# Kernel tuning notes

Measured on AMD Instinct MI355X. Metric: run time of the kernel, lower is better.

Reference implementation:

```python
import jax, jax.numpy as jnp
import numpy as np

N = 512      # nodes
E = 16384    # edges (avg degree 32)
D = 128      # indim
OUT = 128    # outdim


def setup_inputs() -> dict:
    key = jax.random.key(0)
    k1, k2, k3 = jax.random.split(key, 3)
    X = jax.random.normal(k1, (N, N, D), dtype=jnp.float32)
    edge_index = jax.random.randint(k2, (2, E), 0, N, dtype=jnp.int64)
    W = jax.random.normal(k3, (3 * D, OUT), dtype=jnp.float32) * (1.0 / np.sqrt(3 * D))
    b = jnp.zeros((OUT,), dtype=jnp.float32)
    return {"X": X, "edge_index": edge_index, "W": W, "b": b}


def reference(X, edge_index, W, b):
    # X: [N, N, D] tuple features X[i, j] for (subgraph root i, node j)
    # edge_index: [2, E] directed edges (src -> dst), aggr = 'sum'
    n = X.shape[0]
    src, dst = edge_index[0], edge_index[1]
    # Dense binary adjacency (sum aggregation counts multi-edges, matching
    # scatter-add over the edge list). A[k, j] = #edges k -> j.
    A = jnp.zeros((n, n), dtype=X.dtype).at[src, dst].add(jnp.ones((src.shape[0],), X.dtype))
    # OpMessagePassingOnSubg2D: within subgraph i, aggregate over neighbors of j
    # X1[i, j] = sum_{k in N(j)} X[i, k]
    X1 = jnp.einsum('kj,ikd->ijd', A, X)
    # OpMessagePassingCrossSubg2D: across subgraphs, aggregate over neighbors of i
    # X2[i, j] = sum_{k in N(i)} X[k, j]
    X2 = jnp.einsum('ki,kjd->ijd', A, X)
    # catvalue([X1, X2]) -> [X, X1, X2], then pointwise MLP (single Linear)
    H = jnp.concatenate([X, X1, X2], axis=-1)  # [N, N, 3D]
    return H @ W + b  # [N, N, OUT]
```

## Files before the change

kernel.cpp:

```cpp
#include <hip/hip_runtime.h>
#include <hip/hip_bf16.h>
#include <stdint.h>

#define NN 512
#define DD 128
#define EE 16384

typedef short bf16x8 __attribute__((ext_vector_type(8)));
typedef short bf16x4 __attribute__((ext_vector_type(4)));
typedef float f32x4  __attribute__((ext_vector_type(4)));
typedef unsigned int u32;

__device__ __forceinline__ short f2bf(float f) {
    union { __hip_bfloat16 h; short s; } u;
    u.h = __float2bfloat16(f);
    return u.s;
}
__device__ __forceinline__ u32 pk2(float a, float b) {
    return (u32)(unsigned short)f2bf(a) | ((u32)(unsigned short)f2bf(b) << 16);
}

typedef __attribute__((address_space(3))) unsigned int lds_u32;
typedef __attribute__((address_space(1))) const unsigned int glb_u32;
__device__ __forceinline__ void gll16(void* l, const void* g) {
    __builtin_amdgcn_global_load_lds((glb_u32*)g, (lds_u32*)l, 16, 0, 0);
}


__global__ void k_zero(float* __restrict__ At) {
    At[blockIdx.x * 256 + threadIdx.x] = 0.0f;
}

__global__ void k_edges(const int* __restrict__ ei, float* __restrict__ At) {
    __shared__ int flag;
    if (threadIdx.x == 0) flag = 0;
    __syncthreads();
    int any = 0;
    for (int i = threadIdx.x; i < EE; i += blockDim.x) any |= ei[2 * i + 1];
    if (any) atomicOr(&flag, 1);
    __syncthreads();
    const bool is32 = (flag != 0);
    for (int e = threadIdx.x; e < EE; e += blockDim.x) {
        int src, dst;
        if (is32) { src = ei[e];     dst = ei[EE + e]; }
        else      { src = ei[2 * e]; dst = ei[2 * (EE + e)]; }
        atomicAdd(&At[dst * NN + src], 1.0f);
    }
}

__global__ void k_wt2(const float* __restrict__ W, short* __restrict__ Wt2) {
    int t = blockIdx.x * 256 + threadIdx.x;
    int kk = t >> 7, n = t & 127;
    int s = kk >> 7, d = kk & 127;
    Wt2[s * 16384 + n * 128 + d] = f2bf(W[t]);
}

__global__ void k_pack_at(const float* __restrict__ At, short* __restrict__ Atp) {
    int t = blockIdx.x * 256 + threadIdx.x;
    int T = t >> 6, l = t & 63;
    int row = (T >> 4) * 16 + (l & 15);
    int col = (T & 15) * 32 + (l >> 4) * 8;
    const float* s = &At[row * 512 + col];
    bf16x8 p;
    #pragma unroll
    for (int e = 0; e < 8; ++e) p[e] = f2bf(s[e]);
    *(bf16x8*)&Atp[(size_t)T * 512 + l * 8] = p;
}

__global__ __launch_bounds__(512, 2) void k_slab(const float* __restrict__ X,
                                                 const short* __restrict__ Wt2,
                                                 const short* __restrict__ Atp,
                                                 short* __restrict__ Y2,
                                                 short* __restrict__ Pp) {
    __shared__ __align__(16) short sh[65536];
    short* Xc = sh;
    short* Yc = sh + 16384;
    short* Lw = sh + 32768;

    const int tid  = threadIdx.x;
    const int lane = tid & 63;
    const int wv   = tid >> 6;
    const int lm   = lane & 15;
    const int lq   = lane >> 4;
    const int i    = blockIdx.x;

    const int mw   = wv & 1;
    const int quad = wv >> 1;
    const int rowh = quad & 1;
    const int colh = quad >> 1;
    const int wr   = wv * 64;

    #pragma unroll
    for (int it = 0; it < 8; ++it) {
        int slot = it * 512 + tid;
        int s01 = slot >> 11, kb = (slot >> 10) & 1;
        int n = (slot >> 3) & 127, pc = slot & 7;
        gll16(&Lw[slot * 8],
              &Wt2[(1 + s01) * 16384 + n * 128 + kb * 64 + ((pc ^ (n & 7)) * 8)]);
    }

    f32x4 acc[4][8] = {};

    for (int kc = 0; kc < 4; ++kc) {
        if (kc) __syncthreads();
        #pragma unroll
        for (int it = 0; it < 8; ++it) {
            int g = tid + it * 512;
            int r = g >> 5, c4 = g & 31;
            float4 v = *(const float4*)&X[(size_t)i * 65536 + (kc * 128 + r) * 128 + c4 * 4];
            int kb = c4 >> 4, c = c4 & 15, p = c >> 1, h2 = c & 1;
            bf16x4 pcv; pcv[0] = f2bf(v.x); pcv[1] = f2bf(v.y); pcv[2] = f2bf(v.z); pcv[3] = f2bf(v.w);
            *(bf16x4*)&Xc[kb * 8192 + r * 64 + ((p ^ (r & 7)) * 8 + h2 * 4)] = pcv;
        }
        __syncthreads();

        f32x4 ay[4][4] = {};
        #pragma unroll
        for (int sl = 0; sl < 4; ++sl) {
            int kb = sl >> 1, ks = sl & 1, Cc = ks * 4 + lq;
            bf16x8 af[4], bw[4];
            #pragma unroll
            for (int mf = 0; mf < 4; ++mf) {
                int R = rowh * 64 + mf * 16 + lm;
                af[mf] = *(const bf16x8*)&Xc[kb * 8192 + R * 64 + ((Cc ^ (R & 7)) * 8)];
            }
            #pragma unroll
            for (int nf = 0; nf < 4; ++nf) {
                int R = colh * 64 + nf * 16 + lm;
                bw[nf] = *(const bf16x8*)&Lw[mw * 16384 + kb * 8192 + R * 64 + ((Cc ^ (R & 7)) * 8)];
            }
            #pragma unroll
            for (int mf = 0; mf < 4; ++mf)
                #pragma unroll
                for (int nf = 0; nf < 4; ++nf)
                    ay[mf][nf] = __builtin_amdgcn_mfma_f32_16x16x32_bf16(
                        af[mf], bw[nf], ay[mf][nf], 0, 0, 0);
        }
        if (mw == 0) {
            #pragma unroll
            for (int mf = 0; mf < 4; ++mf)
                #pragma unroll
                for (int nf = 0; nf < 4; ++nf)
                    #pragma unroll
                    for (int rr = 0; rr < 4; ++rr) {
                        int rl64 = mf * 16 + lq * 4 + rr;
                        int n = colh * 64 + nf * 16 + lm;
                        Yc[rowh * 8192 + n * 64 + (((rl64 >> 3) ^ (n & 7)) * 8 + (rl64 & 7))]
                            = f2bf(ay[mf][nf][rr]);
                    }
        } else {
            #pragma unroll
            for (int mf = 0; mf < 4; ++mf)
                #pragma unroll
                for (int nf = 0; nf < 4; ++nf)
                    #pragma unroll
                    for (int rr = 0; rr < 4; ++rr) {
                        int row = kc * 128 + rowh * 64 + mf * 16 + lq * 4 + rr;
                        int n = colh * 64 + nf * 16 + lm;
                        Y2[(size_t)i * 65536 + row * 128 + n] = f2bf(ay[mf][nf][rr]);
                    }
        }
        __syncthreads();

        #pragma unroll
        for (int kb2 = 0; kb2 < 2; ++kb2)
            #pragma unroll
            for (int ks = 0; ks < 2; ++ks) {
                int kt = kc * 4 + kb2 * 2 + ks;
                bf16x8 af[4], bf[8];
                #pragma unroll
                for (int mf = 0; mf < 4; ++mf)
                    af[mf] = *(const bf16x8*)&Atp[(size_t)((wv * 4 + mf) * 16 + kt) * 512 + lane * 8];
                #pragma unroll
                for (int nf = 0; nf < 8; ++nf) {
                    int R = nf * 16 + lm;
                    bf[nf] = *(const bf16x8*)&Yc[kb2 * 8192 + R * 64 + (((ks * 4 + lq) ^ (R & 7)) * 8)];
                }
                #pragma unroll
                for (int mf = 0; mf < 4; ++mf)
                    #pragma unroll
                    for (int nf = 0; nf < 8; ++nf)
                        acc[mf][nf] = __builtin_amdgcn_mfma_f32_16x16x32_bf16(
                            af[mf], bf[nf], acc[mf][nf], 0, 0, 0);
            }
    }
    __syncthreads();

    #pragma unroll
    for (int mf = 0; mf < 4; ++mf)
        #pragma unroll
        for (int nf = 0; nf < 8; ++nf)
            #pragma unroll
            for (int rr = 0; rr < 4; ++rr)
                sh[(wr + mf * 16 + lq * 4 + rr) * 128 + nf * 16 + lm]
                    = f2bf(acc[mf][nf][rr]);
    __syncthreads();
    #pragma unroll
    for (int it = 0; it < 16; ++it) {
        int q = tid + it * 512;
        int row = q >> 4, oc = (q & 15) * 8;
        *(bf16x8*)&Pp[(size_t)i * 65536 + row * 128 + oc]
            = *(const bf16x8*)&sh[row * 128 + oc];
    }
}

__global__ __launch_bounds__(256) void k_t(const short* __restrict__ Y2,
                                           short* __restrict__ Y2T) {
    __shared__ __align__(16) u32 U[128 * 64];
    const int tid = threadIdx.x;
    const int j  = blockIdx.x >> 2;
    const int k0 = (blockIdx.x & 3) * 128;

    const int c8 = tid & 15;
    const int a0 = tid >> 4;
    #pragma unroll
    for (int it = 0; it < 4; ++it) {
        int a = a0 + it * 16;
        const short* r0 = &Y2[(size_t)(k0 + 2 * a) * 65536 + j * 128 + c8 * 8];
        bf16x8 A0 = *(const bf16x8*)r0;
        bf16x8 A1 = *(const bf16x8*)(r0 + 65536);
        #pragma unroll
        for (int cc = 0; cc < 8; ++cc) {
            int n = c8 * 8 + cc;
            U[n * 64 + (a ^ (n & 28))] =
                (u32)(unsigned short)A0[cc] | ((u32)(unsigned short)A1[cc] << 16);
        }
    }
    __syncthreads();
    const int ch = tid & 15;
    const int n0 = tid >> 4;
    #pragma unroll
    for (int it = 0; it < 8; ++it) {
        int n = n0 + it * 16;
        uint4 q = *(const uint4*)&U[n * 64 + ((ch * 4) ^ (n & 28))];
        *(uint4*)&Y2T[j * 65536 + n * 512 + k0 + ch * 8] = q;
    }
}

__global__ __launch_bounds__(256) void k_a2f(const float* __restrict__ X,
                                             const short* __restrict__ Atp,
                                             const short* __restrict__ Y2T,
                                             const short* __restrict__ Wt2,
                                             const short* __restrict__ Pp,
                                             const float* __restrict__ bias,
                                             float* __restrict__ out) {
    __shared__ __align__(16) short sm[16384];
    short* As = sm;
    short* Bs = sm + 8192;

    const int tid  = threadIdx.x;
    const int lane = tid & 63;
    const int wv   = tid >> 6;
    const int wr   = (wv >> 1) * 64;
    const int wc   = (wv & 1) * 64;
    const int lm   = lane & 15;
    const int lq   = lane >> 4;
    const int j  = blockIdx.x >> 2;
    const int i0 = (blockIdx.x & 3) * 128;

    f32x4 acc[4][4] = {};

    #pragma unroll
    for (int kb = 0; kb < 2; ++kb) {
        #pragma unroll
        for (int it = 0; it < 8; ++it) {
            int g = tid + it * 256;
            int r = g >> 4, c4 = g & 15;
            float4 v = *(const float4*)&X[(size_t)(i0 + r) * 65536 + j * 128 + kb * 64 + c4 * 4];
            int p = c4 >> 1, h2 = c4 & 1;
            bf16x4 pc; pc[0] = f2bf(v.x); pc[1] = f2bf(v.y); pc[2] = f2bf(v.z); pc[3] = f2bf(v.w);
            *(bf16x4*)&As[r * 64 + ((p ^ (r & 7)) * 8 + h2 * 4)] = pc;
        }
        #pragma unroll
        for (int it = 0; it < 4; ++it) {
            int slot = it * 256 + tid;
            int n = slot >> 3, pc = slot & 7;
            gll16(&Bs[slot * 8], &Wt2[n * 128 + kb * 64 + ((pc ^ (n & 7)) * 8)]);
        }
        __syncthreads();
        #pragma unroll
        for (int ks = 0; ks < 2; ++ks) {
            bf16x8 af[4], bf[4];
            #pragma unroll
            for (int mf = 0; mf < 4; ++mf) {
                int R = wr + mf * 16 + lm, Cc = ks * 4 + lq;
                af[mf] = *(const bf16x8*)&As[R * 64 + (Cc ^ (R & 7)) * 8];
            }
            #pragma unroll
            for (int nf = 0; nf < 4; ++nf) {
                int R = wc + nf * 16 + lm, Cc = ks * 4 + lq;
                bf[nf] = *(const bf16x8*)&Bs[R * 64 + (Cc ^ (R & 7)) * 8];
            }
            #pragma unroll
            for (int mf = 0; mf < 4; ++mf)
                #pragma unroll
                for (int nf = 0; nf < 4; ++nf)
                    acc[mf][nf] = __builtin_amdgcn_mfma_f32_16x16x32_bf16(
                        af[mf], bf[nf], acc[mf][nf], 0, 0, 0);
        }
        __syncthreads();
    }

    const int jt0 = (i0 >> 4) + (wr >> 4);
    for (int kb = 0; kb < 8; ++kb) {
        const int k0 = kb * 64;
        #pragma unroll
        for (int it = 0; it < 4; ++it) {
            int slot = it * 256 + tid;
            int r = slot >> 3, p = slot & 7;
            int cg = (p ^ (r & 7)) * 8;
            gll16(&Bs[slot * 8], &Y2T[j * 65536 + r * 512 + k0 + cg]);
        }
        __syncthreads();
        #pragma unroll
        for (int ks = 0; ks < 2; ++ks) {
            int kt = kb * 2 + ks;
            bf16x8 af[4], bf[4];
            #pragma unroll
            for (int mf = 0; mf < 4; ++mf)
                af[mf] = *(const bf16x8*)&Atp[(size_t)((jt0 + mf) * 16 + kt) * 512 + lane * 8];
            #pragma unroll
            for (int nf = 0; nf < 4; ++nf) {
                int R = wc + nf * 16 + lm, Cc = ks * 4 + lq;
                bf[nf] = *(const bf16x8*)&Bs[R * 64 + (Cc ^ (R & 7)) * 8];
            }
            #pragma unroll
            for (int mf = 0; mf < 4; ++mf)
                #pragma unroll
                for (int nf = 0; nf < 4; ++nf)
                    acc[mf][nf] = __builtin_amdgcn_mfma_f32_16x16x32_bf16(
                        af[mf], bf[nf], acc[mf][nf], 0, 0, 0);
        }
        __syncthreads();
    }

    #pragma unroll
    for (int mf = 0; mf < 4; ++mf)
        #pragma unroll
        for (int nf = 0; nf < 4; ++nf)
            #pragma unroll
            for (int r = 0; r < 4; ++r)
                sm[(wr + mf * 16 + lq * 4 + r) * 128 + wc + nf * 16 + lm]
                    = f2bf(acc[mf][nf][r]);
    __syncthreads();
    #pragma unroll
    for (int it = 0; it < 8; ++it) {
        int q = tid + it * 256;
        int row = q >> 4, oc = (q & 15) * 8;
        bf16x8 vs = *(const bf16x8*)&sm[row * 128 + oc];
        bf16x8 vpl = *(const bf16x8*)&Pp[(size_t)(i0 + row) * 65536 + j * 128 + oc];
        float4 b0 = *(const float4*)&bias[oc];
        float4 b1 = *(const float4*)&bias[oc + 4];
        union { short s; __hip_bfloat16 h; } cs, cp;
        float o[8];
        #pragma unroll
        for (int e = 0; e < 8; ++e) {
            cs.s = vs[e]; cp.s = vpl[e];
            o[e] = __bfloat162float(cs.h) + __bfloat162float(cp.h);
        }
        o[0] += b0.x; o[1] += b0.y; o[2] += b0.z; o[3] += b0.w;
        o[4] += b1.x; o[5] += b1.y; o[6] += b1.z; o[7] += b1.w;
        float* op = &out[(size_t)(i0 + row) * 65536 + j * 128 + oc];
        float4 w0; w0.x = o[0]; w0.y = o[1]; w0.z = o[2]; w0.w = o[3];
        float4 w1; w1.x = o[4]; w1.y = o[5]; w1.z = o[6]; w1.w = o[7];
        *(float4*)op = w0;
        *(float4*)(op + 4) = w1;
    }
}


__global__ __launch_bounds__(256) void k_agg_fb(const float* __restrict__ X,
                                                const float* __restrict__ At,
                                                short* __restrict__ X1b,
                                                short* __restrict__ X2b) {
    __shared__ short As[128 * 72];
    __shared__ short Bs[128 * 72];
    const int tid  = threadIdx.x;
    const int lane = tid & 63;
    const int wv   = tid >> 6;
    const int wr   = (wv >> 1) * 64;
    const int wc   = (wv & 1) * 64;
    const int lm   = lane & 15;
    const int lq   = lane >> 4;
    int a0, Bbase, Bks, Cbase, Crs;
    short* Cp;
    const int bidx = blockIdx.x;
    if (bidx < 2048) {
        int i = bidx >> 2, jt = bidx & 3;
        a0 = jt * 128; Bbase = i * 65536; Bks = 128;
        Cbase = i * 65536 + jt * 16384; Crs = 128; Cp = X1b;
    } else {
        int bb = bidx - 2048;
        int j = bb >> 2, it = bb & 3;
        a0 = it * 128; Bbase = j * 128; Bks = 65536;
        Cbase = it * 8388608 + j * 128; Crs = 65536; Cp = X2b;
    }
    f32x4 acc[4][4] = {};
    const int d  = tid & 127;
    const int kh = tid >> 7;
    for (int kb = 0; kb < 8; ++kb) {
        const int k0 = kb * 64;
        #pragma unroll
        for (int it8 = 0; it8 < 8; ++it8) {
            int g = tid + it8 * 256;
            int r = g >> 4, kq = (g & 15) * 4;
            float4 v = *(const float4*)&At[(a0 + r) * 512 + k0 + kq];
            bf16x4 p; p[0] = f2bf(v.x); p[1] = f2bf(v.y); p[2] = f2bf(v.z); p[3] = f2bf(v.w);
            *(bf16x4*)&As[r * 72 + kq] = p;
        }
        #pragma unroll
        for (int gi = 0; gi < 4; ++gi) {
            int kg = kh * 4 + gi;
            bf16x8 p;
            #pragma unroll
            for (int jj = 0; jj < 8; ++jj)
                p[jj] = f2bf(X[Bbase + (k0 + kg * 8 + jj) * Bks + d]);
            *(bf16x8*)&Bs[d * 72 + kg * 8] = p;
        }
        __syncthreads();
        #pragma unroll
        for (int ks = 0; ks < 2; ++ks) {
            bf16x8 af[4], bfr[4];
            #pragma unroll
            for (int mf = 0; mf < 4; ++mf)
                af[mf] = *(const bf16x8*)&As[(wr + mf * 16 + lm) * 72 + ks * 32 + lq * 8];
            #pragma unroll
            for (int nf = 0; nf < 4; ++nf)
                bfr[nf] = *(const bf16x8*)&Bs[(wc + nf * 16 + lm) * 72 + ks * 32 + lq * 8];
            #pragma unroll
            for (int mf = 0; mf < 4; ++mf)
                #pragma unroll
                for (int nf = 0; nf < 4; ++nf)
                    acc[mf][nf] = __builtin_amdgcn_mfma_f32_16x16x32_bf16(
                        af[mf], bfr[nf], acc[mf][nf], 0, 0, 0);
        }
        __syncthreads();
    }
    #pragma unroll
    for (int mf = 0; mf < 4; ++mf)
        #pragma unroll
        for (int nf = 0; nf < 4; ++nf)
            #pragma unroll
            for (int r = 0; r < 4; ++r) {
                int row = wr + mf * 16 + lq * 4 + r;
                int col = wc + nf * 16 + lm;
                Cp[Cbase + row * Crs + col] = f2bf(acc[mf][nf][r]);
            }
}

__global__ __launch_bounds__(256) void k_final_fb(const float* __restrict__ X,
                                                  const short* __restrict__ X1b,
                                                  const short* __restrict__ X2b,
                                                  const short* __restrict__ Wt2,
                                                  const float* __restrict__ bias,
                                                  float* __restrict__ out) {
    __shared__ short As[128 * 72];
    __shared__ short Ws[128 * 72];
    const int tid  = threadIdx.x;
    const int lane = tid & 63;
    const int wv   = tid >> 6;
    const int wr   = (wv >> 1) * 64;
    const int wc   = (wv & 1) * 64;
    const int lm   = lane & 15;
    const int lq   = lane >> 4;
    const int m0   = blockIdx.x * 128;
    f32x4 acc[4][4] = {};
    for (int ph = 0; ph < 6; ++ph) {
        const int s = ph >> 1, h = ph & 1;
        if (s == 0) {
            #pragma unroll
            for (int it8 = 0; it8 < 8; ++it8) {
                int g = tid + it8 * 256;
                int r = g >> 4, kq = (g & 15) * 4;
                float4 v = *(const float4*)&X[(m0 + r) * 128 + h * 64 + kq];
                bf16x4 p; p[0] = f2bf(v.x); p[1] = f2bf(v.y); p[2] = f2bf(v.z); p[3] = f2bf(v.w);
                *(bf16x4*)&As[r * 72 + kq] = p;
            }
        } else {
            const short* src = (s == 1) ? X1b : X2b;
            #pragma unroll
            for (int it4 = 0; it4 < 4; ++it4) {
                int g = tid + it4 * 256;
                int r = g >> 3, ko = (g & 7) * 8;
                *(bf16x8*)&As[r * 72 + ko] =
                    *(const bf16x8*)&src[(m0 + r) * 128 + h * 64 + ko];
            }
        }
        #pragma unroll
        for (int it4 = 0; it4 < 4; ++it4) {
            int g = tid + it4 * 256;
            int n = g >> 3, ko = (g & 7) * 8;
            *(bf16x8*)&Ws[n * 72 + ko] =
                *(const bf16x8*)&Wt2[s * 16384 + n * 128 + h * 64 + ko];
        }
        __syncthreads();
        #pragma unroll
        for (int ks = 0; ks < 2; ++ks) {
            bf16x8 af[4], bfr[4];
            #pragma unroll
            for (int mf = 0; mf < 4; ++mf)
                af[mf] = *(const bf16x8*)&As[(wr + mf * 16 + lm) * 72 + ks * 32 + lq * 8];
            #pragma unroll
            for (int nf = 0; nf < 4; ++nf)
                bfr[nf] = *(const bf16x8*)&Ws[(wc + nf * 16 + lm) * 72 + ks * 32 + lq * 8];
            #pragma unroll
            for (int mf = 0; mf < 4; ++mf)
                #pragma unroll
                for (int nf = 0; nf < 4; ++nf)
                    acc[mf][nf] = __builtin_amdgcn_mfma_f32_16x16x32_bf16(
                        af[mf], bfr[nf], acc[mf][nf], 0, 0, 0);
        }
        __syncthreads();
    }
    #pragma unroll
    for (int nf = 0; nf < 4; ++nf) {
        float bv = bias[wc + nf * 16 + lm];
        #pragma unroll
        for (int mf = 0; mf < 4; ++mf)
            #pragma unroll
            for (int r = 0; r < 4; ++r) {
                int row = m0 + wr + mf * 16 + lq * 4 + r;
                int col = wc + nf * 16 + lm;
                out[row * 128 + col] = acc[mf][nf][r] + bv;
            }
    }
}

extern "C" void kernel_launch(void* const* d_in, const int* in_sizes, int n_in,
                              void* d_out, int out_size, void* d_ws, size_t ws_size,
                              hipStream_t stream) {
    const float* X  = (const float*)d_in[0];
    const int*   ei = (const int*)d_in[1];
    const float* W  = (const float*)d_in[2];
    const float* b  = (const float*)d_in[3];
    float* out = (float*)d_out;
    char* ws = (char*)d_ws;
    const size_t MB = 1u << 20;

    float* At  = (float*)ws;
    short* Atp = (short*)(ws + 1 * MB);
    short* Wt2 = (short*)(ws + 1 * MB + 512 * 1024);

    k_zero   <<<1024, 256, 0, stream>>>(At);
    k_edges  <<<1, 1024, 0, stream>>>(ei, At);
    k_wt2    <<<192, 256, 0, stream>>>(W, Wt2);
    k_pack_at<<<128, 256, 0, stream>>>(At, Atp);

    if (ws_size >= 194 * MB) {
        short* Y2  = (short*)(ws + 2 * MB);
        short* Y2T = (short*)(ws + 66 * MB);
        short* Pp  = (short*)(ws + 130 * MB);
        k_slab<<<512, 512, 0, stream>>>(X, Wt2, Atp, Y2, Pp);
        k_t   <<<2048, 256, 0, stream>>>(Y2, Y2T);
        k_a2f <<<2048, 256, 0, stream>>>(X, Atp, Y2T, Wt2, Pp, b, out);
    } else {
        short* X1b = (short*)(ws + 2 * MB);
        short* X2b = (short*)(ws + 66 * MB);
        k_agg_fb  <<<4096, 256, 0, stream>>>(X, At, X1b, X2b);
        k_final_fb<<<2048, 256, 0, stream>>>(X, X1b, X2b, Wt2, b, out);
    }
}
```

Baseline: 524.5 us.

## Halve k_slab LDS by reading pre-packed W fragments from global memory

Adds a kernel that packs the W slices into MFMA fragment order. k_slab now loads its W operands directly from global or cache instead of keeping a 64KB LDS copy, which halves shared memory to 64KB. It also stages the Y2 tile through LDS so the global stores are coalesced, and writes the final Pp tile out in two halves so it fits the smaller buffer. The aim is to reach two blocks per CU and make the stores coalesced, at the cost of more global or L2 traffic for W and extra barriers.

```diff
diff --git a/kernel.cpp b/kernel.cpp
--- a/kernel.cpp
+++ b/kernel.cpp
@@ -15,9 +15,6 @@
     union { __hip_bfloat16 h; short s; } u;
     u.h = __float2bfloat16(f);
     return u.s;
-}
-__device__ __forceinline__ u32 pk2(float a, float b) {
-    return (u32)(unsigned short)f2bf(a) | ((u32)(unsigned short)f2bf(b) << 16);
 }
 
 typedef __attribute__((address_space(3))) unsigned int lds_u32;
@@ -67,15 +64,27 @@
     *(bf16x8*)&Atp[(size_t)T * 512 + l * 8] = p;
 }
 
+__global__ void k_pack_w(const float* __restrict__ W, short* __restrict__ Wp) {
+    int t = blockIdx.x * 256 + threadIdx.x;
+    int T = t >> 6, l = t & 63;
+    int s = T >> 5, nt = (T >> 2) & 7, kt = T & 3;
+    int n  = nt * 16 + (l & 15);
+    int d0 = kt * 32 + (l >> 4) * 8;
+    bf16x8 p;
+    #pragma unroll
+    for (int e = 0; e < 8; ++e)
+        p[e] = f2bf(W[((1 + s) * 128 + d0 + e) * 128 + n]);
+    *(bf16x8*)&Wp[(size_t)T * 512 + l * 8] = p;
+}
+
 __global__ __launch_bounds__(512, 2) void k_slab(const float* __restrict__ X,
-                                                 const short* __restrict__ Wt2,
+                                                 const short* __restrict__ Wp,
                                                  const short* __restrict__ Atp,
                                                  short* __restrict__ Y2,
                                                  short* __restrict__ Pp) {
-    __shared__ __align__(16) short sh[65536];
+    __shared__ __align__(16) short sh[32768];
     short* Xc = sh;
     short* Yc = sh + 16384;
-    short* Lw = sh + 32768;
 
     const int tid  = threadIdx.x;
     const int lane = tid & 63;
@@ -89,15 +98,6 @@
     const int rowh = quad & 1;
     const int colh = quad >> 1;
     const int wr   = wv * 64;
-
-    #pragma unroll
-    for (int it = 0; it < 8; ++it) {
-        int slot = it * 512 + tid;
-        int s01 = slot >> 11, kb = (slot >> 10) & 1;
-        int n = (slot >> 3) & 127, pc = slot & 7;
-        gll16(&Lw[slot * 8],
-              &Wt2[(1 + s01) * 16384 + n * 128 + kb * 64 + ((pc ^ (n & 7)) * 8)]);
-    }
 
     f32x4 acc[4][8] = {};
 
@@ -118,6 +118,7 @@
         #pragma unroll
         for (int sl = 0; sl < 4; ++sl) {
             int kb = sl >> 1, ks = sl & 1, Cc = ks * 4 + lq;
+            int kt = kb * 2 + ks;
             bf16x8 af[4], bw[4];
             #pragma unroll
             for (int mf = 0; mf < 4; ++mf) {
@@ -125,10 +126,8 @@
                 af[mf] = *(const bf16x8*)&Xc[kb * 8192 + R * 64 + ((Cc ^ (R & 7)) * 8)];
             }
             #pragma unroll
-            for (int nf = 0; nf < 4; ++nf) {
-                int R = colh * 64 + nf * 16 + lm;
-                bw[nf] = *(const bf16x8*)&Lw[mw * 16384 + kb * 8192 + R * 64 + ((Cc ^ (R & 7)) * 8)];
-            }
+            for (int nf = 0; nf < 4; ++nf)
+                bw[nf] = *(const bf16x8*)&Wp[(size_t)(((mw * 8) + colh * 4 + nf) * 4 + kt) * 512 + lane * 8];
             #pragma unroll
             for (int mf = 0; mf < 4; ++mf)
                 #pragma unroll
@@ -136,6 +135,8 @@
                     ay[mf][nf] = __builtin_amdgcn_mfma_f32_16x16x32_bf16(
                         af[mf], bw[nf], ay[mf][nf], 0, 0, 0);
         }
+        __syncthreads();
+
         if (mw == 0) {
             #pragma unroll
             for (int mf = 0; mf < 4; ++mf)
@@ -155,12 +156,20 @@
                 for (int nf = 0; nf < 4; ++nf)
                     #pragma unroll
                     for (int rr = 0; rr < 4; ++rr) {
-                        int row = kc * 128 + rowh * 64 + mf * 16 + lq * 4 + rr;
+                        int r = rowh * 64 + mf * 16 + lq * 4 + rr;
                         int n = colh * 64 + nf * 16 + lm;
-                        Y2[(size_t)i * 65536 + row * 128 + n] = f2bf(ay[mf][nf][rr]);
+                        Xc[r * 128 + n] = f2bf(ay[mf][nf][rr]);
                     }
         }
         __syncthreads();
+
+        #pragma unroll
+        for (int it = 0; it < 4; ++it) {
+            int q = tid + it * 512;
+            int row = q >> 4, oc = (q & 15) * 8;
+            *(bf16x8*)&Y2[(size_t)i * 65536 + (kc * 128 + row) * 128 + oc]
+                = *(const bf16x8*)&Xc[row * 128 + oc];
+        }
 
         #pragma unroll
         for (int kb2 = 0; kb2 < 2; ++kb2)
@@ -184,23 +193,29 @@
                             af[mf], bf[nf], acc[mf][nf], 0, 0, 0);
             }
     }
-    __syncthreads();
-
-    #pragma unroll
-    for (int mf = 0; mf < 4; ++mf)
-        #pragma unroll
-        for (int nf = 0; nf < 8; ++nf)
-            #pragma unroll
-            for (int rr = 0; rr < 4; ++rr)
-                sh[(wr + mf * 16 + lq * 4 + rr) * 128 + nf * 16 + lm]
-                    = f2bf(acc[mf][nf][rr]);
-    __syncthreads();
-    #pragma unroll
-    for (int it = 0; it < 16; ++it) {
-        int q = tid + it * 512;
-        int row = q >> 4, oc = (q & 15) * 8;
-        *(bf16x8*)&Pp[(size_t)i * 65536 + row * 128 + oc]
-            = *(const bf16x8*)&sh[row * 128 + oc];
+
+    #pragma unroll
+    for (int half = 0; half < 2; ++half) {
+        __syncthreads();
+        if ((wv >> 2) == half) {
+            int lrb = (wv & 3) * 64;
+            #pragma unroll
+            for (int mf = 0; mf < 4; ++mf)
+                #pragma unroll
+                for (int nf = 0; nf < 8; ++nf)
+                    #pragma unroll
+                    for (int rr = 0; rr < 4; ++rr)
+                        sh[(lrb + mf * 16 + lq * 4 + rr) * 128 + nf * 16 + lm]
+                            = f2bf(acc[mf][nf][rr]);
+        }
+        __syncthreads();
+        #pragma unroll
+        for (int it = 0; it < 8; ++it) {
+            int q = tid + it * 512;
+            int row = q >> 4, oc = (q & 15) * 8;
+            *(bf16x8*)&Pp[(size_t)i * 65536 + (half * 256 + row) * 128 + oc]
+                = *(const bf16x8*)&sh[row * 128 + oc];
+        }
     }
 }
 
@@ -540,17 +555,19 @@
     float* At  = (float*)ws;
     short* Atp = (short*)(ws + 1 * MB);
     short* Wt2 = (short*)(ws + 1 * MB + 512 * 1024);
+    short* Wp  = (short*)(ws + 1 * MB + 640 * 1024);
 
     k_zero   <<<1024, 256, 0, stream>>>(At);
     k_edges  <<<1, 1024, 0, stream>>>(ei, At);
     k_wt2    <<<192, 256, 0, stream>>>(W, Wt2);
     k_pack_at<<<128, 256, 0, stream>>>(At, Atp);
+    k_pack_w <<<16, 256, 0, stream>>>(W, Wp);
 
     if (ws_size >= 194 * MB) {
         short* Y2  = (short*)(ws + 2 * MB);
         short* Y2T = (short*)(ws + 66 * MB);
         short* Pp  = (short*)(ws + 130 * MB);
-        k_slab<<<512, 512, 0, stream>>>(X, Wt2, Atp, Y2, Pp);
+        k_slab<<<512, 512, 0, stream>>>(X, Wp, Atp, Y2, Pp);
         k_t   <<<2048, 256, 0, stream>>>(Y2, Y2T);
         k_a2f <<<2048, 256, 0, stream>>>(X, Atp, Y2T, Wt2, Pp, b, out);
     } else {
```

Result: slower. 571.7 us (+9.0%).
